# Performance work log

Hardware: AMD Instinct MI355X
Metric: run time of the kernel (lower is better)

The kernel has to match this reference:

```python
import jax, jax.numpy as jnp
import numpy as np

B, N, D, H = 16, 8192, 1024, 256


def setup_inputs() -> dict:
    key = jax.random.key(0)
    k1, k2, k3 = jax.random.split(key, 3)
    tiles_embeddings = jax.random.normal(k1, (B, N, D), dtype=jnp.float32)
    # Linear(D -> H, bias=False): weight [H, D]
    W1 = jax.random.normal(k2, (H, D), dtype=jnp.float32) * (1.0 / np.sqrt(D))
    # Linear(H -> 1, bias=False): weight [1, H]
    W2 = jax.random.normal(k3, (1, H), dtype=jnp.float32) * (1.0 / np.sqrt(H))
    return {"tiles_embeddings": tiles_embeddings, "W1": W1, "W2": W2}


def reference(tiles_embeddings, W1, W2):
    # attention MLP: Linear -> Tanh -> Linear (no biases)
    h = jnp.tanh(jnp.einsum("bnd,hd->bnh", tiles_embeddings, W1))   # [B, N, H]
    scores = jnp.einsum("bnh,h->bn", h, W2[0])                       # [B, N]
    attn = jax.nn.softmax(scores, axis=-1)                           # softmax over tiles
    out = jnp.einsum("bn,bnd->bd", attn, tiles_embeddings)           # [B, D]
    return out
```

## Files before the change

kernel.cpp:

```cpp
#include <hip/hip_runtime.h>
#include <hip/hip_bf16.h>
#include <stdint.h>

#define Bn 16
#define Nn 8192
#define Dn 1024
#define Hn 256

typedef __attribute__((ext_vector_type(8))) short bf16x8;
typedef __attribute__((ext_vector_type(4))) float f32x4;

__device__ __forceinline__ short f2bf(float f) {
    union { float f; uint32_t u; } v; v.f = f;
    uint32_t u = v.u;
    return (short)((u + 0x7FFFu + ((u >> 16) & 1u)) >> 16);
}

__global__ __launch_bounds__(256) void k_cvt_w1(const float* __restrict__ W1,
                                                short* __restrict__ w1bf) {
    int i = blockIdx.x * 256 + threadIdx.x;
    w1bf[i] = f2bf(W1[i]);
}

#define LSTR 40

__global__ __launch_bounds__(256) void k_scores(const float* __restrict__ X,
                                                const short* __restrict__ w1bf,
                                                const float* __restrict__ W2,
                                                float* __restrict__ scores) {
    __shared__ short xa[64 * LSTR];
    __shared__ short wb[256 * LSTR];
    __shared__ float sc[64];

    const int tid  = threadIdx.x;
    const int wave = tid >> 6;
    const int lane = tid & 63;
    const int quad = lane >> 4;
    const int l16  = lane & 15;

    const long row0 = (long)blockIdx.x * 64;
    const float* xbase = X + row0 * Dn;

    const int sx_row = tid >> 2;
    const int sx_k   = (tid & 3) * 8;

    f32x4 acc[4][4];
#pragma unroll
    for (int mi = 0; mi < 4; ++mi)
#pragma unroll
        for (int ni = 0; ni < 4; ++ni)
            acc[mi][ni] = (f32x4){0.f, 0.f, 0.f, 0.f};

    for (int k0 = 0; k0 < Dn; k0 += 32) {
        {
            const float* src = xbase + (long)sx_row * Dn + k0 + sx_k;
            float4 f0 = *(const float4*)(src);
            float4 f1 = *(const float4*)(src + 4);
            bf16x8 pk;
            pk[0] = f2bf(f0.x); pk[1] = f2bf(f0.y); pk[2] = f2bf(f0.z); pk[3] = f2bf(f0.w);
            pk[4] = f2bf(f1.x); pk[5] = f2bf(f1.y); pk[6] = f2bf(f1.z); pk[7] = f2bf(f1.w);
            *(bf16x8*)(&xa[sx_row * LSTR + sx_k]) = pk;
        }
#pragma unroll
        for (int j = 0; j < 4; ++j) {
            int c  = tid + 256 * j;
            int r  = c >> 2;
            int kk = (c & 3) * 8;
            int4 v = *(const int4*)(w1bf + r * Dn + k0 + kk);
            *(int4*)(&wb[r * LSTR + kk]) = v;
        }
        __syncthreads();

        bf16x8 af[4], bq[4];
#pragma unroll
        for (int mi = 0; mi < 4; ++mi)
            af[mi] = *(const bf16x8*)(&xa[(mi * 16 + l16) * LSTR + quad * 8]);
#pragma unroll
        for (int ni = 0; ni < 4; ++ni)
            bq[ni] = *(const bf16x8*)(&wb[(wave * 64 + ni * 16 + l16) * LSTR + quad * 8]);
#pragma unroll
        for (int mi = 0; mi < 4; ++mi)
#pragma unroll
            for (int ni = 0; ni < 4; ++ni)
                acc[mi][ni] = __builtin_amdgcn_mfma_f32_16x16x32_bf16(af[mi], bq[ni], acc[mi][ni], 0, 0, 0);
        __syncthreads();
    }

    if (tid < 64) sc[tid] = 0.f;
    __syncthreads();

    float w2v[4];
#pragma unroll
    for (int ni = 0; ni < 4; ++ni) w2v[ni] = W2[wave * 64 + ni * 16 + l16];

#pragma unroll
    for (int mi = 0; mi < 4; ++mi) {
#pragma unroll
        for (int r = 0; r < 4; ++r) {
            float p = 0.f;
#pragma unroll
            for (int ni = 0; ni < 4; ++ni)
                p += w2v[ni] * tanhf(acc[mi][ni][r]);
            p += __shfl_xor(p, 1);
            p += __shfl_xor(p, 2);
            p += __shfl_xor(p, 4);
            p += __shfl_xor(p, 8);
            if (l16 == 0) atomicAdd(&sc[mi * 16 + quad * 4 + r], p);
        }
    }
    __syncthreads();
    if (tid < 64) scores[row0 + tid] = sc[tid];
}

__global__ __launch_bounds__(256) void k_softmax(const float* __restrict__ scores,
                                                 float* __restrict__ attn) {
    const int b   = blockIdx.x;
    const int tid = threadIdx.x;
    const float* s = scores + b * Nn;
    __shared__ float red[4];
    __shared__ float red2[4];

    float m = -1e30f;
    for (int i = tid; i < Nn; i += 256) m = fmaxf(m, s[i]);
#pragma unroll
    for (int o = 32; o >= 1; o >>= 1) m = fmaxf(m, __shfl_xor(m, o));
    if ((tid & 63) == 0) red[tid >> 6] = m;
    __syncthreads();
    m = fmaxf(fmaxf(red[0], red[1]), fmaxf(red[2], red[3]));

    float sum = 0.f;
    for (int i = tid; i < Nn; i += 256) sum += expf(s[i] - m);
#pragma unroll
    for (int o = 32; o >= 1; o >>= 1) sum += __shfl_xor(sum, o);
    if ((tid & 63) == 0) red2[tid >> 6] = sum;
    __syncthreads();
    sum = red2[0] + red2[1] + red2[2] + red2[3];

    const float inv = 1.f / sum;
    float* a = attn + b * Nn;
    for (int i = tid; i < Nn; i += 256) a[i] = expf(s[i] - m) * inv;
}

__global__ __launch_bounds__(256) void k_wsum(const float* __restrict__ X,
                                              const float* __restrict__ attn,
                                              float* __restrict__ out) {
    const int b   = blockIdx.y;
    const int c   = blockIdx.x;
    const int tid = threadIdx.x;
    __shared__ float a_s[128];
    if (tid < 128) a_s[tid] = attn[b * Nn + c * 128 + tid];
    __syncthreads();

    const float* xp = X + ((long)b * Nn + (long)c * 128) * Dn + tid * 4;
    float4 acc = make_float4(0.f, 0.f, 0.f, 0.f);
#pragma unroll 4
    for (int n = 0; n < 128; ++n) {
        float4 x = *(const float4*)(xp + (long)n * Dn);
        float a = a_s[n];
        acc.x += a * x.x; acc.y += a * x.y; acc.z += a * x.z; acc.w += a * x.w;
    }
    float* o = out + b * Dn + tid * 4;
    atomicAdd(o + 0, acc.x);
    atomicAdd(o + 1, acc.y);
    atomicAdd(o + 2, acc.z);
    atomicAdd(o + 3, acc.w);
}

extern "C" void kernel_launch(void* const* d_in, const int* in_sizes, int n_in,
                              void* d_out, int out_size, void* d_ws, size_t ws_size,
                              hipStream_t stream) {
    (void)in_sizes; (void)n_in; (void)ws_size;
    const float* X  = (const float*)d_in[0];
    const float* W1 = (const float*)d_in[1];
    const float* W2 = (const float*)d_in[2];
    float* out = (float*)d_out;

    char* ws = (char*)d_ws;
    short* w1bf   = (short*)ws;
    float* scores = (float*)(ws + (1 << 20));
    float* attn   = (float*)(ws + (1 << 20) + (1 << 19));

    hipMemsetAsync(d_out, 0, out_size * sizeof(float), stream);

    k_cvt_w1<<<(Hn * Dn) / 256, 256, 0, stream>>>(W1, w1bf);
    k_scores<<<(Bn * Nn) / 64, 256, 0, stream>>>(X, w1bf, W2, scores);
    k_softmax<<<Bn, 256, 0, stream>>>(scores, attn);
    dim3 g(64, Bn);
    k_wsum<<<g, 256, 0, stream>>>(X, attn, out);
}
```

Measured before the change: 854.2 us.

## Retile score GEMM with swizzled W1 LDS loads, vectorize softmax, replace atomics with reduce

The scores GEMM now uses 128-row tiles with 512 threads and a K step of 64. W1 is pre-converted into a swizzled bf16 layout and copied straight into LDS with global_load_lds, which is meant to cut per-block staging overhead and LDS bank conflicts. tanh is replaced by an exp-based fast approximation, and softmax runs with 1024 threads holding values in registers. The weighted sum writes partials, reversed in block order so it can hit X still resident in cache, and a separate reduce kernel sums them, replacing the output memset and float atomics. The cost is more workspace, an extra launch, and slightly lower accuracy in tanh and exp.

```diff
diff --git a/kernel.cpp b/kernel.cpp
--- a/kernel.cpp
+++ b/kernel.cpp
@@ -11,38 +11,53 @@
 typedef __attribute__((ext_vector_type(4))) float f32x4;
 
 __device__ __forceinline__ short f2bf(float f) {
-    union { float f; uint32_t u; } v; v.f = f;
-    uint32_t u = v.u;
-    return (short)((u + 0x7FFFu + ((u >> 16) & 1u)) >> 16);
+    __hip_bfloat16 h = __float2bfloat16(f);
+    return *reinterpret_cast<short*>(&h);
+}
+
+__device__ __forceinline__ float tanh_fast(float x) {
+    float e = __expf(2.0f * x);
+    return 1.0f - __fdividef(2.0f, 1.0f + e);
 }
 
 __global__ __launch_bounds__(256) void k_cvt_w1(const float* __restrict__ W1,
-                                                short* __restrict__ w1bf) {
-    int i = blockIdx.x * 256 + threadIdx.x;
-    w1bf[i] = f2bf(W1[i]);
-}
-
-#define LSTR 40
-
-__global__ __launch_bounds__(256) void k_scores(const float* __restrict__ X,
-                                                const short* __restrict__ w1bf,
+                                                short* __restrict__ w1s) {
+    int i   = blockIdx.x * 256 + threadIdx.x;
+    int h   = i >> 7;
+    int kk8 = i & 127;
+    int p   = kk8 >> 3;
+    int c8  = kk8 & 7;
+    const float* src = W1 + h * Dn + kk8 * 8;
+    bf16x8 pk;
+#pragma unroll
+    for (int j = 0; j < 8; ++j) pk[j] = f2bf(src[j]);
+    char* dst = (char*)w1s + p * 32768 + h * 128 + ((c8 ^ (h & 7)) << 4);
+    *(bf16x8*)dst = pk;
+}
+
+#define XSTR 72
+
+__global__ __launch_bounds__(512) void k_scores(const float* __restrict__ X,
+                                                const short* __restrict__ w1s,
                                                 const float* __restrict__ W2,
                                                 float* __restrict__ scores) {
-    __shared__ short xa[64 * LSTR];
-    __shared__ short wb[256 * LSTR];
-    __shared__ float sc[64];
+    __shared__ short xa[128 * XSTR];
+    __shared__ short wb[256 * 64];
+    __shared__ float sc[128];
 
     const int tid  = threadIdx.x;
     const int wave = tid >> 6;
     const int lane = tid & 63;
     const int quad = lane >> 4;
     const int l16  = lane & 15;
-
-    const long row0 = (long)blockIdx.x * 64;
+    const int wr   = wave >> 2;
+    const int wc   = wave & 3;
+
+    const long row0 = (long)blockIdx.x * 128;
     const float* xbase = X + row0 * Dn;
 
-    const int sx_row = tid >> 2;
-    const int sx_k   = (tid & 3) * 8;
+    const int srow = tid >> 2;
+    const int sk   = (tid & 3) << 4;
 
     f32x4 acc[4][4];
 #pragma unroll
@@ -51,47 +66,60 @@
         for (int ni = 0; ni < 4; ++ni)
             acc[mi][ni] = (f32x4){0.f, 0.f, 0.f, 0.f};
 
-    for (int k0 = 0; k0 < Dn; k0 += 32) {
+    float w2v[4];
+#pragma unroll
+    for (int ni = 0; ni < 4; ++ni) w2v[ni] = W2[wc * 64 + ni * 16 + l16];
+
+    for (int k0 = 0; k0 < Dn; k0 += 64) {
         {
-            const float* src = xbase + (long)sx_row * Dn + k0 + sx_k;
+            const float* src = xbase + (long)srow * Dn + k0 + sk;
             float4 f0 = *(const float4*)(src);
             float4 f1 = *(const float4*)(src + 4);
-            bf16x8 pk;
-            pk[0] = f2bf(f0.x); pk[1] = f2bf(f0.y); pk[2] = f2bf(f0.z); pk[3] = f2bf(f0.w);
-            pk[4] = f2bf(f1.x); pk[5] = f2bf(f1.y); pk[6] = f2bf(f1.z); pk[7] = f2bf(f1.w);
-            *(bf16x8*)(&xa[sx_row * LSTR + sx_k]) = pk;
-        }
-#pragma unroll
-        for (int j = 0; j < 4; ++j) {
-            int c  = tid + 256 * j;
-            int r  = c >> 2;
-            int kk = (c & 3) * 8;
-            int4 v = *(const int4*)(w1bf + r * Dn + k0 + kk);
-            *(int4*)(&wb[r * LSTR + kk]) = v;
+            float4 f2 = *(const float4*)(src + 8);
+            float4 f3 = *(const float4*)(src + 12);
+            bf16x8 p0, p1;
+            p0[0] = f2bf(f0.x); p0[1] = f2bf(f0.y); p0[2] = f2bf(f0.z); p0[3] = f2bf(f0.w);
+            p0[4] = f2bf(f1.x); p0[5] = f2bf(f1.y); p0[6] = f2bf(f1.z); p0[7] = f2bf(f1.w);
+            p1[0] = f2bf(f2.x); p1[1] = f2bf(f2.y); p1[2] = f2bf(f2.z); p1[3] = f2bf(f2.w);
+            p1[4] = f2bf(f3.x); p1[5] = f2bf(f3.y); p1[6] = f2bf(f3.z); p1[7] = f2bf(f3.w);
+            *(bf16x8*)(&xa[srow * XSTR + sk]) = p0;
+            *(bf16x8*)(&xa[srow * XSTR + sk + 8]) = p1;
+        }
+        {
+            const char* wsrc = (const char*)w1s + ((long)k0 << 9);
+            char* wdst = (char*)wb;
+#pragma unroll
+            for (int j = 0; j < 4; ++j)
+                __builtin_amdgcn_global_load_lds(
+                    (const __attribute__((address_space(1))) unsigned int*)(wsrc + j * 8192 + tid * 16),
+                    (__attribute__((address_space(3))) unsigned int*)(wdst + j * 8192 + tid * 16),
+                    16, 0, 0);
         }
         __syncthreads();
 
-        bf16x8 af[4], bq[4];
-#pragma unroll
-        for (int mi = 0; mi < 4; ++mi)
-            af[mi] = *(const bf16x8*)(&xa[(mi * 16 + l16) * LSTR + quad * 8]);
-#pragma unroll
-        for (int ni = 0; ni < 4; ++ni)
-            bq[ni] = *(const bf16x8*)(&wb[(wave * 64 + ni * 16 + l16) * LSTR + quad * 8]);
-#pragma unroll
-        for (int mi = 0; mi < 4; ++mi)
-#pragma unroll
-            for (int ni = 0; ni < 4; ++ni)
-                acc[mi][ni] = __builtin_amdgcn_mfma_f32_16x16x32_bf16(af[mi], bq[ni], acc[mi][ni], 0, 0, 0);
+#pragma unroll
+        for (int ks = 0; ks < 2; ++ks) {
+            bf16x8 af[4], bq[4];
+#pragma unroll
+            for (int mi = 0; mi < 4; ++mi)
+                af[mi] = *(const bf16x8*)(&xa[(wr * 64 + mi * 16 + l16) * XSTR + ks * 32 + quad * 8]);
+#pragma unroll
+            for (int ni = 0; ni < 4; ++ni) {
+                int rw    = wc * 64 + ni * 16 + l16;
+                int byteo = (rw * 128 + ks * 64 + quad * 16) ^ ((rw & 7) << 4);
+                bq[ni] = *(const bf16x8*)((const char*)wb + byteo);
+            }
+#pragma unroll
+            for (int mi = 0; mi < 4; ++mi)
+#pragma unroll
+                for (int ni = 0; ni < 4; ++ni)
+                    acc[mi][ni] = __builtin_amdgcn_mfma_f32_16x16x32_bf16(af[mi], bq[ni], acc[mi][ni], 0, 0, 0);
+        }
         __syncthreads();
     }
 
-    if (tid < 64) sc[tid] = 0.f;
-    __syncthreads();
-
-    float w2v[4];
-#pragma unroll
-    for (int ni = 0; ni < 4; ++ni) w2v[ni] = W2[wave * 64 + ni * 16 + l16];
+    if (tid < 128) sc[tid] = 0.f;
+    __syncthreads();
 
 #pragma unroll
     for (int mi = 0; mi < 4; ++mi) {
@@ -100,53 +128,69 @@
             float p = 0.f;
 #pragma unroll
             for (int ni = 0; ni < 4; ++ni)
-                p += w2v[ni] * tanhf(acc[mi][ni][r]);
+                p += w2v[ni] * tanh_fast(acc[mi][ni][r]);
             p += __shfl_xor(p, 1);
             p += __shfl_xor(p, 2);
             p += __shfl_xor(p, 4);
             p += __shfl_xor(p, 8);
-            if (l16 == 0) atomicAdd(&sc[mi * 16 + quad * 4 + r], p);
+            if (l16 == 0) atomicAdd(&sc[wr * 64 + mi * 16 + quad * 4 + r], p);
         }
     }
     __syncthreads();
-    if (tid < 64) scores[row0 + tid] = sc[tid];
-}
-
-__global__ __launch_bounds__(256) void k_softmax(const float* __restrict__ scores,
-                                                 float* __restrict__ attn) {
+    if (tid < 128) scores[row0 + tid] = sc[tid];
+}
+
+__global__ __launch_bounds__(1024) void k_softmax(const float* __restrict__ scores,
+                                                  float* __restrict__ attn) {
     const int b   = blockIdx.x;
     const int tid = threadIdx.x;
     const float* s = scores + b * Nn;
-    __shared__ float red[4];
-    __shared__ float red2[4];
-
-    float m = -1e30f;
-    for (int i = tid; i < Nn; i += 256) m = fmaxf(m, s[i]);
+    __shared__ float redm[16];
+    __shared__ float reds[16];
+
+    float4 v0 = ((const float4*)s)[tid * 2];
+    float4 v1 = ((const float4*)s)[tid * 2 + 1];
+
+    float m = fmaxf(fmaxf(fmaxf(v0.x, v0.y), fmaxf(v0.z, v0.w)),
+                    fmaxf(fmaxf(v1.x, v1.y), fmaxf(v1.z, v1.w)));
 #pragma unroll
     for (int o = 32; o >= 1; o >>= 1) m = fmaxf(m, __shfl_xor(m, o));
-    if ((tid & 63) == 0) red[tid >> 6] = m;
-    __syncthreads();
-    m = fmaxf(fmaxf(red[0], red[1]), fmaxf(red[2], red[3]));
-
-    float sum = 0.f;
-    for (int i = tid; i < Nn; i += 256) sum += expf(s[i] - m);
+    if ((tid & 63) == 0) redm[tid >> 6] = m;
+    __syncthreads();
+    m = redm[0];
+#pragma unroll
+    for (int i = 1; i < 16; ++i) m = fmaxf(m, redm[i]);
+
+    float e[8];
+    e[0] = __expf(v0.x - m); e[1] = __expf(v0.y - m);
+    e[2] = __expf(v0.z - m); e[3] = __expf(v0.w - m);
+    e[4] = __expf(v1.x - m); e[5] = __expf(v1.y - m);
+    e[6] = __expf(v1.z - m); e[7] = __expf(v1.w - m);
+    float sum = ((e[0] + e[1]) + (e[2] + e[3])) + ((e[4] + e[5]) + (e[6] + e[7]));
 #pragma unroll
     for (int o = 32; o >= 1; o >>= 1) sum += __shfl_xor(sum, o);
-    if ((tid & 63) == 0) red2[tid >> 6] = sum;
-    __syncthreads();
-    sum = red2[0] + red2[1] + red2[2] + red2[3];
-
-    const float inv = 1.f / sum;
+    if ((tid & 63) == 0) reds[tid >> 6] = sum;
+    __syncthreads();
+    float tot = 0.f;
+#pragma unroll
+    for (int i = 0; i < 16; ++i) tot += reds[i];
+    const float inv = 1.0f / tot;
+
     float* a = attn + b * Nn;
-    for (int i = tid; i < Nn; i += 256) a[i] = expf(s[i] - m) * inv;
+    float4 o0 = make_float4(e[0] * inv, e[1] * inv, e[2] * inv, e[3] * inv);
+    float4 o1 = make_float4(e[4] * inv, e[5] * inv, e[6] * inv, e[7] * inv);
+    ((float4*)a)[tid * 2]     = o0;
+    ((float4*)a)[tid * 2 + 1] = o1;
 }
 
 __global__ __launch_bounds__(256) void k_wsum(const float* __restrict__ X,
                                               const float* __restrict__ attn,
-                                              float* __restrict__ out) {
-    const int b   = blockIdx.y;
-    const int c   = blockIdx.x;
-    const int tid = threadIdx.x;
+                                              float* __restrict__ part) {
+    const int slot = blockIdx.y * 64 + blockIdx.x;
+    const int flat = 1023 - slot;
+    const int b    = flat >> 6;
+    const int c    = flat & 63;
+    const int tid  = threadIdx.x;
     __shared__ float a_s[128];
     if (tid < 128) a_s[tid] = attn[b * Nn + c * 128 + tid];
     __syncthreads();
@@ -159,32 +203,40 @@
         float a = a_s[n];
         acc.x += a * x.x; acc.y += a * x.y; acc.z += a * x.z; acc.w += a * x.w;
     }
-    float* o = out + b * Dn + tid * 4;
-    atomicAdd(o + 0, acc.x);
-    atomicAdd(o + 1, acc.y);
-    atomicAdd(o + 2, acc.z);
-    atomicAdd(o + 3, acc.w);
+    *(float4*)(part + (long)flat * Dn + tid * 4) = acc;
+}
+
+__global__ __launch_bounds__(256) void k_reduce(const float* __restrict__ part,
+                                                float* __restrict__ out) {
+    int i = blockIdx.x * 256 + threadIdx.x;
+    int b = i >> 10;
+    int d = i & 1023;
+    const float* p = part + (long)b * 64 * Dn + d;
+    float s = 0.f;
+#pragma unroll 8
+    for (int c = 0; c < 64; ++c) s += p[c * Dn];
+    out[i] = s;
 }
 
 extern "C" void kernel_launch(void* const* d_in, const int* in_sizes, int n_in,
                               void* d_out, int out_size, void* d_ws, size_t ws_size,
                               hipStream_t stream) {
-    (void)in_sizes; (void)n_in; (void)ws_size;
+    (void)in_sizes; (void)n_in; (void)ws_size; (void)out_size;
     const float* X  = (const float*)d_in[0];
     const float* W1 = (const float*)d_in[1];
     const float* W2 = (const float*)d_in[2];
     float* out = (float*)d_out;
 
     char* ws = (char*)d_ws;
-    short* w1bf   = (short*)ws;
-    float* scores = (float*)(ws + (1 << 20));
-    float* attn   = (float*)(ws + (1 << 20) + (1 << 19));
-
-    hipMemsetAsync(d_out, 0, out_size * sizeof(float), stream);
-
-    k_cvt_w1<<<(Hn * Dn) / 256, 256, 0, stream>>>(W1, w1bf);
-    k_scores<<<(Bn * Nn) / 64, 256, 0, stream>>>(X, w1bf, W2, scores);
-    k_softmax<<<Bn, 256, 0, stream>>>(scores, attn);
+    short* w1s    = (short*)ws;
+    float* scores = (float*)(ws + (1 << 19));
+    float* attn   = (float*)(ws + (2 << 19));
+    float* part   = (float*)(ws + (3 << 19));
+
+    k_cvt_w1<<<(Hn * Dn) / 8 / 256, 256, 0, stream>>>(W1, w1s);
+    k_scores<<<(Bn * Nn) / 128, 512, 0, stream>>>(X, w1s, W2, scores);
+    k_softmax<<<Bn, 1024, 0, stream>>>(scores, attn);
     dim3 g(64, Bn);
-    k_wsum<<<g, 256, 0, stream>>>(X, attn, out);
-}
+    k_wsum<<<g, 256, 0, stream>>>(X, attn, part);
+    k_reduce<<<64, 256, 0, stream>>>(part, out);
+}
```

Measured after the change: 810.9 us. -5.1%, faster.
